# Kernel tuning notes

Measured on AMD Instinct MI355X. Metric: run time of the kernel, lower is better.

The kernel has to match this reference:

```python
import jax, jax.numpy as jnp
import numpy as np
from functools import partial

N = 50000
IN_C, HID_C, OUT_C = 256, 128, 64
E = 800000


def gcn_norm(src, dst, n_nodes):
    # PyG gcn_norm with unit edge weights: deg from target index, D^-1/2 A D^-1/2
    ones = jnp.ones(src.shape[0], dtype=jnp.float32)
    deg = jax.ops.segment_sum(ones, dst, num_segments=n_nodes)
    dinv = jnp.where(deg > 0, jax.lax.rsqrt(deg), 0.0)
    return dinv[src] * dinv[dst]


def gcn_conv(x, src, dst, norm, W, b):
    h = x @ W                              # [N, out] dense GEMM first (PyG order)
    msg = h[src] * norm[:, None]           # gather + scale  [E', out]
    out = jax.ops.segment_sum(msg, dst, num_segments=x.shape[0])
    return out + b


def setup_inputs() -> dict:
    key = jax.random.key(0)
    ks = jax.random.split(key, 6)
    x = jax.random.normal(ks[0], (N, IN_C), dtype=jnp.float32)
    edge_index = jax.random.randint(ks[1], (2, E), 0, N, dtype=jnp.int32)
    # Glorot-ish init for weights
    W1 = jax.random.normal(ks[2], (IN_C, HID_C), dtype=jnp.float32) / np.sqrt(IN_C)
    b1 = jnp.zeros((HID_C,), dtype=jnp.float32)
    W2 = jax.random.normal(ks[3], (HID_C, OUT_C), dtype=jnp.float32) / np.sqrt(HID_C)
    b2 = jnp.zeros((OUT_C,), dtype=jnp.float32)
    return {"x": x, "edge_index": edge_index, "W1": W1, "b1": b1, "W2": W2, "b2": b2}


def reference(x, edge_index, W1, b1, W2, b2):
    # eval mode: dropout is identity
    n = x.shape[0]
    loop = jnp.arange(n, dtype=edge_index.dtype)
    src = jnp.concatenate([edge_index[0], loop])   # add self loops (static E+N)
    dst = jnp.concatenate([edge_index[1], loop])
    norm = gcn_norm(src, dst, n)
    h = jax.nn.relu(gcn_conv(x, src, dst, norm, W1, b1))
    return gcn_conv(h, src, dst, norm, W2, b2)
```

## Files before the change

kernel.cpp:

```cpp
#include <hip/hip_runtime.h>


#define TPB 256
#define NBKT 196
#define EB_CAP 4608
#define CSR_CAP 6400
#define P1_EPB 8192

typedef __bf16 bf16x8 __attribute__((ext_vector_type(8)));
typedef __bf16 bf16x4 __attribute__((ext_vector_type(4)));
typedef __bf16 bf16x2 __attribute__((ext_vector_type(2)));
typedef float f32x4 __attribute__((ext_vector_type(4)));

__device__ __forceinline__ float bflo(unsigned u) { return __uint_as_float(u << 16); }
__device__ __forceinline__ float bfhi(unsigned u) { return __uint_as_float(u & 0xffff0000u); }

__global__ __launch_bounds__(256) void clear_wprep_kernel(
    unsigned* __restrict__ gcnt, float* __restrict__ dinv, __bf16* __restrict__ h2s,
    int N,
    const float* __restrict__ W1, const float* __restrict__ W2,
    __bf16* __restrict__ wf1, __bf16* __restrict__ wf2) {
    if (blockIdx.x == 0) {
        int t = threadIdx.x;
        if (t < NBKT) gcnt[t] = 0;
        if (t == 0) dinv[N] = 0.0f;
        if (t < 32) ((unsigned*)(h2s + (long)N * 64))[t] = 0u;
        return;
    }
    int g = (blockIdx.x - 1) * TPB + threadIdx.x;
    if (g < 64 * 64) {
        int frag = g >> 6, L = g & 63;
        int kstep = frag >> 3, oct = frag & 7;
        int oc = oct * 16 + (L & 15);
        int k0 = kstep * 32 + (L >> 4) * 8;
        bf16x8 v;
#pragma unroll
        for (int j = 0; j < 8; j++) v[j] = (__bf16)W1[(k0 + j) * 128 + oc];
        ((bf16x8*)wf1)[g] = v;
    } else if (g < 64 * 64 + 16 * 64) {
        int g2 = g - 64 * 64;
        int frag = g2 >> 6, L = g2 & 63;
        int kstep = frag >> 2, oct = frag & 3;
        int oc = oct * 16 + (L & 15);
        int k0 = kstep * 32 + (L >> 4) * 8;
        bf16x8 v;
#pragma unroll
        for (int j = 0; j < 8; j++) v[j] = (__bf16)W2[(k0 + j) * 64 + oc];
        ((bf16x8*)wf2)[g2] = v;
    }
}

template <bool IN_BF16, int K, int OC, bool SCALE>
__device__ __forceinline__ void gemm_body(int bid, int tid, const void* __restrict__ Ain,
                                          const bf16x8* __restrict__ wfrag,
                                          const float* __restrict__ dinv,
                                          __bf16* __restrict__ outp, int M) {
    constexpr int KS = K / 32, OT = OC / 16;
    int wave = tid >> 6, lane = tid & 63;
    int col = lane & 15, q = lane >> 4;
    long rb = (long)bid * 128 + wave * 32;
    long r0 = rb + col, r1 = rb + 16 + col;
    long r0c = (r0 < M) ? r0 : (M - 1);
    long r1c = (r1 < M) ? r1 : (M - 1);

    f32x4 acc[OT][2];
#pragma unroll
    for (int o = 0; o < OT; o++) {
        acc[o][0] = (f32x4){0.f, 0.f, 0.f, 0.f};
        acc[o][1] = (f32x4){0.f, 0.f, 0.f, 0.f};
    }

#pragma unroll
    for (int ks = 0; ks < KS; ks++) {
        int k0 = ks * 32 + q * 8;
        bf16x8 b0, b1;
        if constexpr (IN_BF16) {
            const __bf16* A = (const __bf16*)Ain;
            b0 = *(const bf16x8*)(A + r0c * K + k0);
            b1 = *(const bf16x8*)(A + r1c * K + k0);
        } else {
            const float* A = (const float*)Ain;
            float4 f0a = *(const float4*)(A + r0c * K + k0);
            float4 f0b = *(const float4*)(A + r0c * K + k0 + 4);
            float4 f1a = *(const float4*)(A + r1c * K + k0);
            float4 f1b = *(const float4*)(A + r1c * K + k0 + 4);
            b0[0] = (__bf16)f0a.x; b0[1] = (__bf16)f0a.y; b0[2] = (__bf16)f0a.z; b0[3] = (__bf16)f0a.w;
            b0[4] = (__bf16)f0b.x; b0[5] = (__bf16)f0b.y; b0[6] = (__bf16)f0b.z; b0[7] = (__bf16)f0b.w;
            b1[0] = (__bf16)f1a.x; b1[1] = (__bf16)f1a.y; b1[2] = (__bf16)f1a.z; b1[3] = (__bf16)f1a.w;
            b1[4] = (__bf16)f1b.x; b1[5] = (__bf16)f1b.y; b1[6] = (__bf16)f1b.z; b1[7] = (__bf16)f1b.w;
        }
#pragma unroll
        for (int ot = 0; ot < OT; ot++) {
            bf16x8 a = wfrag[(ks * OT + ot) * 64 + lane];
            acc[ot][0] = __builtin_amdgcn_mfma_f32_16x16x32_bf16(a, b0, acc[ot][0], 0, 0, 0);
            acc[ot][1] = __builtin_amdgcn_mfma_f32_16x16x32_bf16(a, b1, acc[ot][1], 0, 0, 0);
        }
    }

    float sc0 = 1.f, sc1 = 1.f;
    if constexpr (SCALE) {
        sc0 = dinv[r0c];
        sc1 = dinv[r1c];
    }
#pragma unroll
    for (int ot = 0; ot < OT; ot++) {
        int oc = ot * 16 + q * 4;
        if (r0 < M) {
            bf16x4 v;
#pragma unroll
            for (int r = 0; r < 4; r++) v[r] = (__bf16)(acc[ot][0][r] * sc0);
            *(bf16x4*)(outp + r0 * OC + oc) = v;
        }
        if (r1 < M) {
            bf16x4 v;
#pragma unroll
            for (int r = 0; r < 4; r++) v[r] = (__bf16)(acc[ot][1][r] * sc1);
            *(bf16x4*)(outp + r1 * OC + oc) = v;
        }
    }
}

__global__ __launch_bounds__(256) void p1_gemm1_kernel(
    const int* __restrict__ src, const int* __restrict__ dst, int E, int p1Blocks,
    unsigned* __restrict__ gcnt, unsigned* __restrict__ ebuf,
    const float* __restrict__ x, const bf16x8* __restrict__ wf1,
    __bf16* __restrict__ h1u, int M) {
    __shared__ unsigned sPacked[P1_EPB];
    __shared__ int sCnt[256];
    if ((int)blockIdx.x < p1Blocks) {
        int t = threadIdx.x;
        sCnt[t] = 0;
        __syncthreads();
        long e0 = (long)blockIdx.x * P1_EPB;
        int cnt = (int)(E - e0);
        if (cnt > P1_EPB) cnt = P1_EPB;
        for (int i = t; i < cnt; i += 256) {
            unsigned s = (unsigned)src[e0 + i];
            unsigned d = (unsigned)dst[e0 + i];
            sPacked[i] = (s << 16) | d;
            atomicAdd(&sCnt[d >> 8], 1);
        }
        __syncthreads();
        int base = 0;
        if (t < NBKT) base = (int)atomicAdd(&gcnt[t], (unsigned)sCnt[t]);
        __syncthreads();
        if (t < NBKT) sCnt[t] = t * EB_CAP + base;
        __syncthreads();
        for (int i = t; i < cnt; i += 256) {
            unsigned p = sPacked[i];
            int b = (int)((p & 0xffffu) >> 8);
            int pos = atomicAdd(&sCnt[b], 1);
            if (pos < (b + 1) * EB_CAP) ebuf[pos] = p;
        }
    } else {
        gemm_body<false, 256, 128, false>(blockIdx.x - p1Blocks, threadIdx.x,
                                          x, wf1, nullptr, h1u, M);
    }
}

__global__ __launch_bounds__(256) void csr_kernel(
    const unsigned* __restrict__ gcnt, const unsigned* __restrict__ ebuf,
    int* __restrict__ csr, int2* __restrict__ se, float* __restrict__ dinv, int N) {
    __shared__ unsigned sEdges[EB_CAP];
    __shared__ int sCnt[256];
    __shared__ int sScan[256];
    int b = blockIdx.x, t = threadIdx.x;
    int m = (int)gcnt[b];
    if (m > EB_CAP) m = EB_CAP;
    sCnt[t] = 0;
    __syncthreads();
    const unsigned* eb = ebuf + b * EB_CAP;
    for (int i = t; i < m; i += 256) {
        unsigned p = eb[i];
        sEdges[i] = p;
        atomicAdd(&sCnt[p & 255u], 1);
    }
    __syncthreads();
    int c = sCnt[t];
    int pad = (c + 7) & ~7;
    sScan[t] = pad;
    __syncthreads();
    for (int off = 1; off < 256; off <<= 1) {
        int v = (t >= off) ? sScan[t - off] : 0;
        __syncthreads();
        sScan[t] += v;
        __syncthreads();
    }
    int start = b * CSR_CAP + sScan[t] - pad;
    int node = (b << 8) + t;
    if (node < N) {
        se[node] = make_int2(start, start + pad);
        dinv[node] = rsqrtf((float)c + 1.0f);
    }
    __syncthreads();
    sCnt[t] = start;
    __syncthreads();
    for (int i = t; i < m; i += 256) {
        unsigned p = sEdges[i];
        int pos = atomicAdd(&sCnt[p & 255u], 1);
        csr[pos] = (int)(p >> 16);
    }
    if (node < N) {
        for (int k = start + c; k < start + pad; k++) csr[k] = N;
    }
}

#define ACC8()                                             \
    do {                                                   \
        a0x += bflo(v0) * w0; a0y += bfhi(v0) * w0;        \
        a1x += bflo(v1) * w1; a1y += bfhi(v1) * w1;        \
        a2x += bflo(v2) * w2; a2y += bfhi(v2) * w2;        \
        a3x += bflo(v3) * w3; a3y += bfhi(v3) * w3;        \
        a0x += bflo(v4) * w4; a0y += bfhi(v4) * w4;        \
        a1x += bflo(v5) * w5; a1y += bfhi(v5) * w5;        \
        a2x += bflo(v6) * w6; a2y += bfhi(v6) * w6;        \
        a3x += bflo(v7) * w7; a3y += bfhi(v7) * w7;        \
    } while (0)

__global__ __launch_bounds__(256) void agg128_kernel(const __bf16* __restrict__ h,
                                                     const int* __restrict__ csr,
                                                     const int2* __restrict__ se,
                                                     const float* __restrict__ dinv,
                                                     const float* __restrict__ bias,
                                                     __bf16* __restrict__ outp, int N) {
    int gid = blockIdx.x * TPB + threadIdx.x;
    int n = gid >> 6, lane = gid & 63;
    if (n >= N) return;
    int2 s_e = se[n];
    int start = s_e.x, m = s_e.y - s_e.x;
    float dn = dinv[n];
    const unsigned* hp = (const unsigned*)h;
    const int* sl = csr + start;
    unsigned self = hp[(long)n * 64 + lane];
    float a0x = bflo(self) * dn, a0y = bfhi(self) * dn;
    float a1x = 0.f, a1y = 0.f, a2x = 0.f, a2y = 0.f, a3x = 0.f, a3y = 0.f;
    if (m > 0) {
        int4 c0 = *(const int4*)sl;
        int4 c1 = *(const int4*)(sl + 4);
        int i0 = __builtin_amdgcn_readfirstlane(c0.x);
        int i1 = __builtin_amdgcn_readfirstlane(c0.y);
        int i2 = __builtin_amdgcn_readfirstlane(c0.z);
        int i3 = __builtin_amdgcn_readfirstlane(c0.w);
        int i4 = __builtin_amdgcn_readfirstlane(c1.x);
        int i5 = __builtin_amdgcn_readfirstlane(c1.y);
        int i6 = __builtin_amdgcn_readfirstlane(c1.z);
        int i7 = __builtin_amdgcn_readfirstlane(c1.w);
        unsigned v0 = hp[(long)i0 * 64 + lane], v1 = hp[(long)i1 * 64 + lane];
        unsigned v2 = hp[(long)i2 * 64 + lane], v3 = hp[(long)i3 * 64 + lane];
        unsigned v4 = hp[(long)i4 * 64 + lane], v5 = hp[(long)i5 * 64 + lane];
        unsigned v6 = hp[(long)i6 * 64 + lane], v7 = hp[(long)i7 * 64 + lane];
        float w0 = dinv[i0], w1 = dinv[i1], w2 = dinv[i2], w3 = dinv[i3];
        float w4 = dinv[i4], w5 = dinv[i5], w6 = dinv[i6], w7 = dinv[i7];
        int4 d0 = *(const int4*)(sl + 8);
        int4 d1 = *(const int4*)(sl + 12);
        for (int j = 8; j < m; j += 8) {
            int t0 = __builtin_amdgcn_readfirstlane(d0.x);
            int t1 = __builtin_amdgcn_readfirstlane(d0.y);
            int t2 = __builtin_amdgcn_readfirstlane(d0.z);
            int t3 = __builtin_amdgcn_readfirstlane(d0.w);
            int t4 = __builtin_amdgcn_readfirstlane(d1.x);
            int t5 = __builtin_amdgcn_readfirstlane(d1.y);
            int t6 = __builtin_amdgcn_readfirstlane(d1.z);
            int t7 = __builtin_amdgcn_readfirstlane(d1.w);
            unsigned u0 = hp[(long)t0 * 64 + lane], u1 = hp[(long)t1 * 64 + lane];
            unsigned u2 = hp[(long)t2 * 64 + lane], u3 = hp[(long)t3 * 64 + lane];
            unsigned u4 = hp[(long)t4 * 64 + lane], u5 = hp[(long)t5 * 64 + lane];
            unsigned u6 = hp[(long)t6 * 64 + lane], u7 = hp[(long)t7 * 64 + lane];
            float q0 = dinv[t0], q1 = dinv[t1], q2 = dinv[t2], q3 = dinv[t3];
            float q4 = dinv[t4], q5 = dinv[t5], q6 = dinv[t6], q7 = dinv[t7];
            d0 = *(const int4*)(sl + j + 8);
            d1 = *(const int4*)(sl + j + 12);
            ACC8();
            v0 = u0; v1 = u1; v2 = u2; v3 = u3; v4 = u4; v5 = u5; v6 = u6; v7 = u7;
            w0 = q0; w1 = q1; w2 = q2; w3 = q3; w4 = q4; w5 = q5; w6 = q6; w7 = q7;
        }
        ACC8();
    }
    float2 bv = ((const float2*)bias)[lane];
    float ox = (a0x + a1x + a2x + a3x) * dn + bv.x;
    float oy = (a0y + a1y + a2y + a3y) * dn + bv.y;
    ox = fmaxf(ox, 0.f);
    oy = fmaxf(oy, 0.f);
    bf16x2 st = {(__bf16)ox, (__bf16)oy};
    ((bf16x2*)outp)[(long)n * 64 + lane] = st;
}
#undef ACC8

__global__ __launch_bounds__(256) void mfma_gemm2_kernel(const __bf16* __restrict__ Ain,
                                                         const bf16x8* __restrict__ wfrag,
                                                         const float* __restrict__ dinv,
                                                         __bf16* __restrict__ outp, int M) {
    gemm_body<true, 128, 64, true>(blockIdx.x, threadIdx.x, Ain, wfrag, dinv, outp, M);
}

#define ACC8B()                                                                            \
    do {                                                                                   \
        a0 += __uint_as_float((unsigned)v0 << 16); a1 += __uint_as_float((unsigned)v1 << 16); \
        a2 += __uint_as_float((unsigned)v2 << 16); a3 += __uint_as_float((unsigned)v3 << 16); \
        a0 += __uint_as_float((unsigned)v4 << 16); a1 += __uint_as_float((unsigned)v5 << 16); \
        a2 += __uint_as_float((unsigned)v6 << 16); a3 += __uint_as_float((unsigned)v7 << 16); \
    } while (0)

__global__ __launch_bounds__(256) void agg64_kernel(const __bf16* __restrict__ hs,
                                                    const int* __restrict__ csr,
                                                    const int2* __restrict__ se,
                                                    const float* __restrict__ dinv,
                                                    const float* __restrict__ bias,
                                                    float* __restrict__ outp, int N) {
    int gid = blockIdx.x * TPB + threadIdx.x;
    int n = gid >> 6, lane = gid & 63;
    if (n >= N) return;
    int2 s_e = se[n];
    int start = s_e.x, m = s_e.y - s_e.x;
    float dn = dinv[n];
    const unsigned short* hp = (const unsigned short*)hs;
    const int* sl = csr + start;
    float a0 = __uint_as_float(((unsigned)hp[(long)n * 64 + lane]) << 16);
    float a1 = 0.f, a2 = 0.f, a3 = 0.f;
    if (m > 0) {
        int4 c0 = *(const int4*)sl;
        int4 c1 = *(const int4*)(sl + 4);
        int i0 = __builtin_amdgcn_readfirstlane(c0.x);
        int i1 = __builtin_amdgcn_readfirstlane(c0.y);
        int i2 = __builtin_amdgcn_readfirstlane(c0.z);
        int i3 = __builtin_amdgcn_readfirstlane(c0.w);
        int i4 = __builtin_amdgcn_readfirstlane(c1.x);
        int i5 = __builtin_amdgcn_readfirstlane(c1.y);
        int i6 = __builtin_amdgcn_readfirstlane(c1.z);
        int i7 = __builtin_amdgcn_readfirstlane(c1.w);
        unsigned short v0 = hp[(long)i0 * 64 + lane], v1 = hp[(long)i1 * 64 + lane];
        unsigned short v2 = hp[(long)i2 * 64 + lane], v3 = hp[(long)i3 * 64 + lane];
        unsigned short v4 = hp[(long)i4 * 64 + lane], v5 = hp[(long)i5 * 64 + lane];
        unsigned short v6 = hp[(long)i6 * 64 + lane], v7 = hp[(long)i7 * 64 + lane];
        int4 d0 = *(const int4*)(sl + 8);
        int4 d1 = *(const int4*)(sl + 12);
        for (int j = 8; j < m; j += 8) {
            int t0 = __builtin_amdgcn_readfirstlane(d0.x);
            int t1 = __builtin_amdgcn_readfirstlane(d0.y);
            int t2 = __builtin_amdgcn_readfirstlane(d0.z);
            int t3 = __builtin_amdgcn_readfirstlane(d0.w);
            int t4 = __builtin_amdgcn_readfirstlane(d1.x);
            int t5 = __builtin_amdgcn_readfirstlane(d1.y);
            int t6 = __builtin_amdgcn_readfirstlane(d1.z);
            int t7 = __builtin_amdgcn_readfirstlane(d1.w);
            unsigned short u0 = hp[(long)t0 * 64 + lane], u1 = hp[(long)t1 * 64 + lane];
            unsigned short u2 = hp[(long)t2 * 64 + lane], u3 = hp[(long)t3 * 64 + lane];
            unsigned short u4 = hp[(long)t4 * 64 + lane], u5 = hp[(long)t5 * 64 + lane];
            unsigned short u6 = hp[(long)t6 * 64 + lane], u7 = hp[(long)t7 * 64 + lane];
            d0 = *(const int4*)(sl + j + 8);
            d1 = *(const int4*)(sl + j + 12);
            ACC8B();
            v0 = u0; v1 = u1; v2 = u2; v3 = u3; v4 = u4; v5 = u5; v6 = u6; v7 = u7;
        }
        ACC8B();
    }
    outp[(long)n * 64 + lane] = (a0 + a1 + a2 + a3) * dn + bias[lane];
}
#undef ACC8B

static inline int cdiv(long a, long b) { return (int)((a + b - 1) / b); }

extern "C" void kernel_launch(void* const* d_in, const int* in_sizes, int n_in,
                              void* d_out, int out_size, void* d_ws, size_t ws_size,
                              hipStream_t stream) {
    const float* x  = (const float*)d_in[0];
    const int*   ei = (const int*)d_in[1];
    const float* W1 = (const float*)d_in[2];
    const float* b1 = (const float*)d_in[3];
    const float* W2 = (const float*)d_in[4];
    const float* b2 = (const float*)d_in[5];

    const int IN_C = 256;
    const int N = in_sizes[0] / IN_C;
    const int E = in_sizes[1] / 2;
    const int* src = ei;
    const int* dst = ei + E;

    char* w = (char*)d_ws;
    size_t off = 0;
    auto alloc = [&](size_t bytes) { void* p = w + off; off = (off + bytes + 255) & ~255ull; return p; };
    __bf16*   h1u  = (__bf16*)alloc((size_t)(N + 1) * 128 * 2);
    __bf16*   agg1 = (__bf16*)alloc((size_t)N * 128 * 2);
    __bf16*   h2s  = (__bf16*)alloc((size_t)(N + 1) * 64 * 2);
    unsigned* ebuf = (unsigned*)alloc((size_t)NBKT * EB_CAP * 4);
    int*      csr  = (int*)alloc((size_t)NBKT * CSR_CAP * 4);
    int2*     se   = (int2*)alloc((size_t)N * 8);
    float*    dinv = (float*)alloc((size_t)(N + 1) * 4);
    unsigned* gcnt = (unsigned*)alloc(NBKT * 4);
    __bf16*   wf1  = (__bf16*)alloc(64 * 64 * 8 * 2);
    __bf16*   wf2  = (__bf16*)alloc(16 * 64 * 8 * 2);

    int wprepBlocks = cdiv(64 * 64 + 16 * 64, TPB);
    clear_wprep_kernel<<<1 + wprepBlocks, TPB, 0, stream>>>(gcnt, dinv, h2s, N,
                                                            W1, W2, wf1, wf2);

    int p1Blocks = cdiv(E, P1_EPB);
    int gemmBlocks = cdiv(N, 128);
    p1_gemm1_kernel<<<p1Blocks + gemmBlocks, TPB, 0, stream>>>(
        src, dst, E, p1Blocks, gcnt, ebuf, x, (const bf16x8*)wf1, h1u, N);

    csr_kernel<<<NBKT, TPB, 0, stream>>>(gcnt, ebuf, csr, se, dinv, N);

    agg128_kernel<<<cdiv((long)N * 64, TPB), TPB, 0, stream>>>(h1u, csr, se, dinv, b1, agg1, N);

    mfma_gemm2_kernel<<<gemmBlocks, TPB, 0, stream>>>(agg1, (const bf16x8*)wf2, dinv, h2s, N);

    agg64_kernel<<<cdiv((long)N * 64, TPB), TPB, 0, stream>>>(h2s, csr, se, dinv, b2,
                                                              (float*)d_out, N);
}
```

Measured before the change: 184.4 us.

## Fuse layer-1 aggregation with layer-2 MFMA GEMM via per-wave LDS stash

Merges the 128-channel aggregation kernel and the second GEMM into one kernel. Each wave aggregates 16 nodes one after another, stores the bf16 activations in LDS, then runs a 16x64x128 MFMA against the prepacked W2 fragments and writes scaled h2s directly. This drops the agg1 intermediate buffer (its global write and reread) and one kernel launch. In exchange each wave processes its 16 nodes serially, and the grid shrinks to N/64 blocks, so there is less parallelism available to hide gather latency.

```diff
diff --git a/kernel.cpp b/kernel.cpp
--- a/kernel.cpp
+++ b/kernel.cpp
@@ -217,81 +217,107 @@
         a3x += bflo(v7) * w7; a3y += bfhi(v7) * w7;        \
     } while (0)
 
-__global__ __launch_bounds__(256) void agg128_kernel(const __bf16* __restrict__ h,
-                                                     const int* __restrict__ csr,
-                                                     const int2* __restrict__ se,
-                                                     const float* __restrict__ dinv,
-                                                     const float* __restrict__ bias,
-                                                     __bf16* __restrict__ outp, int N) {
-    int gid = blockIdx.x * TPB + threadIdx.x;
-    int n = gid >> 6, lane = gid & 63;
-    if (n >= N) return;
-    int2 s_e = se[n];
-    int start = s_e.x, m = s_e.y - s_e.x;
-    float dn = dinv[n];
-    const unsigned* hp = (const unsigned*)h;
-    const int* sl = csr + start;
-    unsigned self = hp[(long)n * 64 + lane];
-    float a0x = bflo(self) * dn, a0y = bfhi(self) * dn;
-    float a1x = 0.f, a1y = 0.f, a2x = 0.f, a2y = 0.f, a3x = 0.f, a3y = 0.f;
-    if (m > 0) {
-        int4 c0 = *(const int4*)sl;
-        int4 c1 = *(const int4*)(sl + 4);
-        int i0 = __builtin_amdgcn_readfirstlane(c0.x);
-        int i1 = __builtin_amdgcn_readfirstlane(c0.y);
-        int i2 = __builtin_amdgcn_readfirstlane(c0.z);
-        int i3 = __builtin_amdgcn_readfirstlane(c0.w);
-        int i4 = __builtin_amdgcn_readfirstlane(c1.x);
-        int i5 = __builtin_amdgcn_readfirstlane(c1.y);
-        int i6 = __builtin_amdgcn_readfirstlane(c1.z);
-        int i7 = __builtin_amdgcn_readfirstlane(c1.w);
-        unsigned v0 = hp[(long)i0 * 64 + lane], v1 = hp[(long)i1 * 64 + lane];
-        unsigned v2 = hp[(long)i2 * 64 + lane], v3 = hp[(long)i3 * 64 + lane];
-        unsigned v4 = hp[(long)i4 * 64 + lane], v5 = hp[(long)i5 * 64 + lane];
-        unsigned v6 = hp[(long)i6 * 64 + lane], v7 = hp[(long)i7 * 64 + lane];
-        float w0 = dinv[i0], w1 = dinv[i1], w2 = dinv[i2], w3 = dinv[i3];
-        float w4 = dinv[i4], w5 = dinv[i5], w6 = dinv[i6], w7 = dinv[i7];
-        int4 d0 = *(const int4*)(sl + 8);
-        int4 d1 = *(const int4*)(sl + 12);
-        for (int j = 8; j < m; j += 8) {
-            int t0 = __builtin_amdgcn_readfirstlane(d0.x);
-            int t1 = __builtin_amdgcn_readfirstlane(d0.y);
-            int t2 = __builtin_amdgcn_readfirstlane(d0.z);
-            int t3 = __builtin_amdgcn_readfirstlane(d0.w);
-            int t4 = __builtin_amdgcn_readfirstlane(d1.x);
-            int t5 = __builtin_amdgcn_readfirstlane(d1.y);
-            int t6 = __builtin_amdgcn_readfirstlane(d1.z);
-            int t7 = __builtin_amdgcn_readfirstlane(d1.w);
-            unsigned u0 = hp[(long)t0 * 64 + lane], u1 = hp[(long)t1 * 64 + lane];
-            unsigned u2 = hp[(long)t2 * 64 + lane], u3 = hp[(long)t3 * 64 + lane];
-            unsigned u4 = hp[(long)t4 * 64 + lane], u5 = hp[(long)t5 * 64 + lane];
-            unsigned u6 = hp[(long)t6 * 64 + lane], u7 = hp[(long)t7 * 64 + lane];
-            float q0 = dinv[t0], q1 = dinv[t1], q2 = dinv[t2], q3 = dinv[t3];
-            float q4 = dinv[t4], q5 = dinv[t5], q6 = dinv[t6], q7 = dinv[t7];
-            d0 = *(const int4*)(sl + j + 8);
-            d1 = *(const int4*)(sl + j + 12);
-            ACC8();
-            v0 = u0; v1 = u1; v2 = u2; v3 = u3; v4 = u4; v5 = u5; v6 = u6; v7 = u7;
-            w0 = q0; w1 = q1; w2 = q2; w3 = q3; w4 = q4; w5 = q5; w6 = q6; w7 = q7;
-        }
-        ACC8();
-    }
-    float2 bv = ((const float2*)bias)[lane];
-    float ox = (a0x + a1x + a2x + a3x) * dn + bv.x;
-    float oy = (a0y + a1y + a2y + a3y) * dn + bv.y;
-    ox = fmaxf(ox, 0.f);
-    oy = fmaxf(oy, 0.f);
-    bf16x2 st = {(__bf16)ox, (__bf16)oy};
-    ((bf16x2*)outp)[(long)n * 64 + lane] = st;
+__global__ __launch_bounds__(256) void agg128_gemm2_kernel(
+    const __bf16* __restrict__ h, const int* __restrict__ csr,
+    const int2* __restrict__ se, const float* __restrict__ dinv,
+    const float* __restrict__ bias, const bf16x8* __restrict__ wf2,
+    __bf16* __restrict__ h2s, int N) {
+    __shared__ __bf16 stash[4][16 * 132];
+    int wave = threadIdx.x >> 6, lane = threadIdx.x & 63;
+    int n0 = blockIdx.x * 64 + wave * 16;
+    unsigned* stw = (unsigned*)stash[wave];
+
+    for (int i = 0; i < 16; i++) {
+        int n = n0 + i;
+        float ox = 0.f, oy = 0.f;
+        if (n < N) {
+            int2 s_e = se[n];
+            int start = s_e.x, m = s_e.y - s_e.x;
+            float dn = dinv[n];
+            const unsigned* hp = (const unsigned*)h;
+            const int* sl = csr + start;
+            unsigned self = hp[(long)n * 64 + lane];
+            float a0x = bflo(self) * dn, a0y = bfhi(self) * dn;
+            float a1x = 0.f, a1y = 0.f, a2x = 0.f, a2y = 0.f, a3x = 0.f, a3y = 0.f;
+            if (m > 0) {
+                int4 c0 = *(const int4*)sl;
+                int4 c1 = *(const int4*)(sl + 4);
+                int i0 = __builtin_amdgcn_readfirstlane(c0.x);
+                int i1 = __builtin_amdgcn_readfirstlane(c0.y);
+                int i2 = __builtin_amdgcn_readfirstlane(c0.z);
+                int i3 = __builtin_amdgcn_readfirstlane(c0.w);
+                int i4 = __builtin_amdgcn_readfirstlane(c1.x);
+                int i5 = __builtin_amdgcn_readfirstlane(c1.y);
+                int i6 = __builtin_amdgcn_readfirstlane(c1.z);
+                int i7 = __builtin_amdgcn_readfirstlane(c1.w);
+                unsigned v0 = hp[(long)i0 * 64 + lane], v1 = hp[(long)i1 * 64 + lane];
+                unsigned v2 = hp[(long)i2 * 64 + lane], v3 = hp[(long)i3 * 64 + lane];
+                unsigned v4 = hp[(long)i4 * 64 + lane], v5 = hp[(long)i5 * 64 + lane];
+                unsigned v6 = hp[(long)i6 * 64 + lane], v7 = hp[(long)i7 * 64 + lane];
+                float w0 = dinv[i0], w1 = dinv[i1], w2 = dinv[i2], w3 = dinv[i3];
+                float w4 = dinv[i4], w5 = dinv[i5], w6 = dinv[i6], w7 = dinv[i7];
+                int4 d0 = *(const int4*)(sl + 8);
+                int4 d1 = *(const int4*)(sl + 12);
+                for (int j = 8; j < m; j += 8) {
+                    int t0 = __builtin_amdgcn_readfirstlane(d0.x);
+                    int t1 = __builtin_amdgcn_readfirstlane(d0.y);
+                    int t2 = __builtin_amdgcn_readfirstlane(d0.z);
+                    int t3 = __builtin_amdgcn_readfirstlane(d0.w);
+                    int t4 = __builtin_amdgcn_readfirstlane(d1.x);
+                    int t5 = __builtin_amdgcn_readfirstlane(d1.y);
+                    int t6 = __builtin_amdgcn_readfirstlane(d1.z);
+                    int t7 = __builtin_amdgcn_readfirstlane(d1.w);
+                    unsigned u0 = hp[(long)t0 * 64 + lane], u1 = hp[(long)t1 * 64 + lane];
+                    unsigned u2 = hp[(long)t2 * 64 + lane], u3 = hp[(long)t3 * 64 + lane];
+                    unsigned u4 = hp[(long)t4 * 64 + lane], u5 = hp[(long)t5 * 64 + lane];
+                    unsigned u6 = hp[(long)t6 * 64 + lane], u7 = hp[(long)t7 * 64 + lane];
+                    float q0 = dinv[t0], q1 = dinv[t1], q2 = dinv[t2], q3 = dinv[t3];
+                    float q4 = dinv[t4], q5 = dinv[t5], q6 = dinv[t6], q7 = dinv[t7];
+                    d0 = *(const int4*)(sl + j + 8);
+                    d1 = *(const int4*)(sl + j + 12);
+                    ACC8();
+                    v0 = u0; v1 = u1; v2 = u2; v3 = u3; v4 = u4; v5 = u5; v6 = u6; v7 = u7;
+                    w0 = q0; w1 = q1; w2 = q2; w3 = q3; w4 = q4; w5 = q5; w6 = q6; w7 = q7;
+                }
+                ACC8();
+            }
+            float2 bv = ((const float2*)bias)[lane];
+            ox = fmaxf((a0x + a1x + a2x + a3x) * dn + bv.x, 0.f);
+            oy = fmaxf((a0y + a1y + a2y + a3y) * dn + bv.y, 0.f);
+        }
+        bf16x2 st = {(__bf16)ox, (__bf16)oy};
+        stw[i * 66 + lane] = *(unsigned*)&st;
+    }
+
+    int col = lane & 15, q = lane >> 4;
+    const __bf16* srow = stash[wave] + col * 132;
+    f32x4 acc[4];
+#pragma unroll
+    for (int ot = 0; ot < 4; ot++) acc[ot] = (f32x4){0.f, 0.f, 0.f, 0.f};
+#pragma unroll
+    for (int ks = 0; ks < 4; ks++) {
+        bf16x8 bb = *(const bf16x8*)(srow + ks * 32 + q * 8);
+#pragma unroll
+        for (int ot = 0; ot < 4; ot++) {
+            bf16x8 a = wf2[(ks * 4 + ot) * 64 + lane];
+            acc[ot] = __builtin_amdgcn_mfma_f32_16x16x32_bf16(a, bb, acc[ot], 0, 0, 0);
+        }
+    }
+    int node = n0 + col;
+    bool valid = node < N;
+    float dn2 = valid ? dinv[node] : 0.f;
+#pragma unroll
+    for (int ot = 0; ot < 4; ot++) {
+        int oc = ot * 16 + q * 4;
+        if (valid) {
+            bf16x4 v;
+#pragma unroll
+            for (int r = 0; r < 4; r++) v[r] = (__bf16)(acc[ot][r] * dn2);
+            *(bf16x4*)(h2s + (long)node * 64 + oc) = v;
+        }
+    }
 }
 #undef ACC8
-
-__global__ __launch_bounds__(256) void mfma_gemm2_kernel(const __bf16* __restrict__ Ain,
-                                                         const bf16x8* __restrict__ wfrag,
-                                                         const float* __restrict__ dinv,
-                                                         __bf16* __restrict__ outp, int M) {
-    gemm_body<true, 128, 64, true>(blockIdx.x, threadIdx.x, Ain, wfrag, dinv, outp, M);
-}
 
 #define ACC8B()                                                                            \
     do {                                                                                   \
@@ -380,7 +406,6 @@
     size_t off = 0;
     auto alloc = [&](size_t bytes) { void* p = w + off; off = (off + bytes + 255) & ~255ull; return p; };
     __bf16*   h1u  = (__bf16*)alloc((size_t)(N + 1) * 128 * 2);
-    __bf16*   agg1 = (__bf16*)alloc((size_t)N * 128 * 2);
     __bf16*   h2s  = (__bf16*)alloc((size_t)(N + 1) * 64 * 2);
     unsigned* ebuf = (unsigned*)alloc((size_t)NBKT * EB_CAP * 4);
     int*      csr  = (int*)alloc((size_t)NBKT * CSR_CAP * 4);
@@ -401,9 +426,8 @@
 
     csr_kernel<<<NBKT, TPB, 0, stream>>>(gcnt, ebuf, csr, se, dinv, N);
 
-    agg128_kernel<<<cdiv((long)N * 64, TPB), TPB, 0, stream>>>(h1u, csr, se, dinv, b1, agg1, N);
-
-    mfma_gemm2_kernel<<<gemmBlocks, TPB, 0, stream>>>(agg1, (const bf16x8*)wf2, dinv, h2s, N);
+    agg128_gemm2_kernel<<<cdiv(N, 64), TPB, 0, stream>>>(h1u, csr, se, dinv, b1,
+                                                         (const bf16x8*)wf2, h2s, N);
 
     agg64_kernel<<<cdiv((long)N * 64, TPB), TPB, 0, stream>>>(h2s, csr, se, dinv, b2,
                                                               (float*)d_out, N);
```

Result: slower. 193.3 us (+4.8%).
